# Kernel optimization log

Measured on AMD Instinct MI355X. Metric: run time of the kernel, lower is better.

Reference implementation:

```python
import jax, jax.numpy as jnp
import numpy as np

QLEN, MLEN, BSZ, DMODEL, NHEAD, DHEAD = 512, 512, 8, 1024, 16, 64
KLEN = QLEN + MLEN
LN_EPS = 1e-5


def layer_norm(x, g, b):
    mu = jnp.mean(x, axis=-1, keepdims=True)
    var = jnp.var(x, axis=-1, keepdims=True)
    return (x - mu) / jnp.sqrt(var + LN_EPS) * g + b


def rel_shift(x):
    # x: [qlen, klen, bsz, n_head] -- Transformer-XL relative shift trick
    q, k, b, n = x.shape
    x_pad = jnp.pad(x, ((0, 0), (1, 0), (0, 0), (0, 0)))  # zero col at front of dim 1
    x_pad = x_pad.reshape(k + 1, q, b, n)
    return x_pad[1:].reshape(q, k, b, n)


def setup_inputs() -> dict:
    key = jax.random.key(0)
    ks = jax.random.split(key, 10)
    w = lambda k, shape: (jax.random.normal(k, shape, jnp.float32) * 0.02)
    return {
        "content": jax.random.normal(ks[0], (QLEN, BSZ, DMODEL), jnp.float32),
        "mems": jax.random.normal(ks[1], (MLEN, BSZ, DMODEL), jnp.float32),
        "r": jax.random.normal(ks[2], (KLEN, DMODEL), jnp.float32),
        "q_bias": w(ks[3], (NHEAD, DHEAD)),
        "mask": jnp.zeros((QLEN, KLEN, BSZ), jnp.bool_),
        "W_q": w(ks[4], (NHEAD * DHEAD, DMODEL)),
        "W_kv": w(ks[5], (2 * NHEAD * DHEAD, DMODEL)),
        "W_r": w(ks[6], (NHEAD * DHEAD, DMODEL)),
        "b_r": jnp.zeros((NHEAD * DHEAD,), jnp.float32),
        "W_o": w(ks[7], (DMODEL, NHEAD * DHEAD)),
        "b_o": jnp.zeros((DMODEL,), jnp.float32),
        "ln_g": jnp.ones((DMODEL,), jnp.float32),
        "ln_b": jnp.zeros((DMODEL,), jnp.float32),
    }


def reference(content, mems, r, q_bias, mask, W_q, W_kv, W_r, b_r, W_o, b_o, ln_g, ln_b):
    Q, B, D = content.shape
    H, Dh = q_bias.shape
    scale = 1.0 / (Dh ** 0.5)

    c = layer_norm(content, ln_g, ln_b)          # [Q,B,D]
    m = layer_norm(mems, ln_g, ln_b)             # [M,B,D]
    cat = jnp.concatenate([m, c], axis=0)        # [K,B,D]
    K = cat.shape[0]

    kv = cat @ W_kv.T                            # [K,B,2*H*Dh]
    k, v = jnp.split(kv, 2, axis=-1)
    k = k.reshape(K, B, H, Dh)
    v = v.reshape(K, B, H, Dh)

    q = (c @ W_q.T).reshape(Q, B, H, Dh) + q_bias  # [Q,B,H,Dh]
    rproj = (r @ W_r.T + b_r).reshape(K, H, Dh)    # [K,H,Dh]

    AC = jnp.einsum('ibnd,jbnd->ijbn', q, k)       # content-content
    BD = rel_shift(jnp.einsum('ibnd,jnd->ijbn', q, rproj))  # content-position
    score = (AC + BD) * scale                      # [Q,K,B,H]
    score = jnp.where(mask[..., None], -jnp.inf, score)
    prob = jax.nn.softmax(score, axis=1)

    vec = jnp.einsum('ijbn,jbnd->ibnd', prob, v).reshape(Q, B, H * Dh)
    attn_out = vec @ W_o.T + b_o                   # [Q,B,D]
    # IdentityResidualGate: x + relu(y) with x = layer-normed content
    return c + jax.nn.relu(attn_out)
```

## Files before the change

### kernel.cpp

```cpp
#include <hip/hip_runtime.h>
#include <hip/hip_bf16.h>
#include <math.h>

#define QLEN 512
#define MLENC 512
#define KLEN 1024
#define BSZ 8
#define DMODEL 1024
#define NHEAD 16
#define DHEAD 64

typedef __hip_bfloat16 bf16;
typedef unsigned short u16;
typedef unsigned int u32;
typedef __attribute__((ext_vector_type(8))) short s16x8;
typedef __attribute__((ext_vector_type(4))) float f32x4;

#define MFMA16(a, b, c) __builtin_amdgcn_mfma_f32_16x16x32_bf16(a, b, c, 0, 0, 0)

static __device__ __forceinline__ float b2f(bf16 x) { return __bfloat162float(x); }
static __device__ __forceinline__ bf16 f2b(float x) { return __float2bfloat16(x); }
static __device__ __forceinline__ u16 bbu(float x) {
    bf16 h = __float2bfloat16(x);
    return *reinterpret_cast<u16*>(&h);
}
static __device__ __forceinline__ float sh2f(u16 v) {
    return __uint_as_float(((u32)v) << 16);
}

static __device__ __forceinline__ void gl_lds16(const void* g, void* l) {
    __builtin_amdgcn_global_load_lds(
        (const __attribute__((address_space(1))) void*)g,
        (__attribute__((address_space(3))) void*)l, 16, 0, 0);
}

__global__ __launch_bounds__(256) void wconv_kernel(const float* __restrict__ wq,
                                                    const float* __restrict__ wkv,
                                                    const float* __restrict__ wr,
                                                    const float* __restrict__ wo,
                                                    bf16* __restrict__ out) {
    int off = (blockIdx.x * 256 + threadIdx.x) * 8;
    const float* src;
    if (off < 1048576)       src = wq + off;
    else if (off < 3145728)  src = wkv + (off - 1048576);
    else if (off < 4194304)  src = wr + (off - 3145728);
    else                     src = wo + (off - 4194304);
    float4 f0 = *(const float4*)src;
    float4 f1 = *(const float4*)(src + 4);
    s16x8 v;
    v[0] = (short)bbu(f0.x); v[1] = (short)bbu(f0.y);
    v[2] = (short)bbu(f0.z); v[3] = (short)bbu(f0.w);
    v[4] = (short)bbu(f1.x); v[5] = (short)bbu(f1.y);
    v[6] = (short)bbu(f1.z); v[7] = (short)bbu(f1.w);
    *(s16x8*)((short*)out + off) = v;
}

__global__ __launch_bounds__(256) void ln_kernel(const float* __restrict__ content,
                                                 const float* __restrict__ mems,
                                                 const float* __restrict__ g,
                                                 const float* __restrict__ bet,
                                                 bf16* __restrict__ cat) {
    int row = blockIdx.x;
    int tid = threadIdx.x;
    const float* src = (row < MLENC * BSZ)
        ? mems + (size_t)row * DMODEL
        : content + (size_t)(row - MLENC * BSZ) * DMODEL;

    float x[4];
    float s = 0.f, ss = 0.f;
#pragma unroll
    for (int l = 0; l < 4; ++l) {
        int d = l * 256 + tid;
        x[l] = src[d];
        s += x[l];
        ss += x[l] * x[l];
    }
#pragma unroll
    for (int off = 32; off > 0; off >>= 1) {
        s  += __shfl_xor(s, off);
        ss += __shfl_xor(ss, off);
    }
    __shared__ float red[8];
    int wid = tid >> 6;
    if ((tid & 63) == 0) { red[wid * 2] = s; red[wid * 2 + 1] = ss; }
    __syncthreads();
    s  = red[0] + red[2] + red[4] + red[6];
    ss = red[1] + red[3] + red[5] + red[7];
    float mu  = s * (1.f / DMODEL);
    float var = ss * (1.f / DMODEL) - mu * mu;
    float rs  = rsqrtf(var + 1e-5f);
    bf16* dst = cat + (size_t)row * DMODEL;
#pragma unroll
    for (int l = 0; l < 4; ++l) {
        int d = l * 256 + tid;
        dst[d] = f2b((x[l] - mu) * rs * g[d] + bet[d]);
    }
}

template <int MODE, bool AF32, bool BF32>
__global__ __launch_bounds__(256) void gemm_mfma(const void* __restrict__ Av,
                                                 const void* __restrict__ Bv,
                                                 const float* __restrict__ bias,
                                                 const bf16* __restrict__ resid,
                                                 bf16* __restrict__ Cb,
                                                 float* __restrict__ Cf,
                                                 int Mr, int N) {
    __shared__ short As[128 * 32];
    __shared__ short Bs[128 * 32];

    int m0 = blockIdx.y * 128, n0 = blockIdx.x * 128;
    int tid = threadIdx.x;
    int w = tid >> 6, lane = tid & 63, l15 = lane & 15, quad = lane >> 4;
    int wm = w & 1, wn = w >> 1;

    const short* Ab = (const short*)Av;
    const float* Af = (const float*)Av;
    const short* Bb = (const short*)Bv;
    const float* Bf = (const float*)Bv;

    f32x4 acc[4][4];
#pragma unroll
    for (int i = 0; i < 4; ++i)
#pragma unroll
        for (int j = 0; j < 4; ++j) acc[i][j] = (f32x4){0.f, 0.f, 0.f, 0.f};

    for (int kt = 0; kt < 1024; kt += 32) {
        __syncthreads();
        if (!AF32) {
#pragma unroll
            for (int li = 0; li < 2; ++li) {
                int id = (li * 4 + w) * 64 + lane;
                int row = id >> 2, kc = (id & 3) * 8;
                gl_lds16(Ab + ((size_t)(m0 + row) * 1024 + kt + kc),
                         &As[(li * 4 + w) * 512]);
            }
        } else {
            int m = tid >> 1, kc = (tid & 1) * 16;
            const float* src = Af + (size_t)(m0 + m) * 1024 + kt + kc;
            u32* dst = (u32*)&As[m * 32 + kc];
#pragma unroll
            for (int q2 = 0; q2 < 4; ++q2) {
                float4 f = *(const float4*)(src + q2 * 4);
                dst[q2 * 2]     = ((u32)bbu(f.y) << 16) | bbu(f.x);
                dst[q2 * 2 + 1] = ((u32)bbu(f.w) << 16) | bbu(f.z);
            }
        }
        if (!BF32) {
#pragma unroll
            for (int li = 0; li < 2; ++li) {
                int id = (li * 4 + w) * 64 + lane;
                int row = id >> 2, kc = (id & 3) * 8;
                gl_lds16(Bb + ((size_t)(n0 + row) * 1024 + kt + kc),
                         &Bs[(li * 4 + w) * 512]);
            }
        } else {
            int nn = tid >> 1, kc = (tid & 1) * 16;
            const float* src = Bf + (size_t)(n0 + nn) * 1024 + kt + kc;
            u32* dst = (u32*)&Bs[nn * 32 + kc];
#pragma unroll
            for (int q2 = 0; q2 < 4; ++q2) {
                float4 f = *(const float4*)(src + q2 * 4);
                dst[q2 * 2]     = ((u32)bbu(f.y) << 16) | bbu(f.x);
                dst[q2 * 2 + 1] = ((u32)bbu(f.w) << 16) | bbu(f.z);
            }
        }
        __syncthreads();

        s16x8 af[4], bfr[4];
#pragma unroll
        for (int mb = 0; mb < 4; ++mb)
            af[mb] = *(const s16x8*)&As[(wm * 64 + mb * 16 + l15) * 32 + quad * 8];
#pragma unroll
        for (int nb = 0; nb < 4; ++nb)
            bfr[nb] = *(const s16x8*)&Bs[(wn * 64 + nb * 16 + l15) * 32 + quad * 8];
#pragma unroll
        for (int mb = 0; mb < 4; ++mb)
#pragma unroll
            for (int nb = 0; nb < 4; ++nb)
                acc[mb][nb] = MFMA16(af[mb], bfr[nb], acc[mb][nb]);
    }

#pragma unroll
    for (int mb = 0; mb < 4; ++mb) {
#pragma unroll
        for (int nb = 0; nb < 4; ++nb) {
#pragma unroll
            for (int r = 0; r < 4; ++r) {
                int m = m0 + wm * 64 + mb * 16 + quad * 4 + r;
                int col = n0 + wn * 64 + nb * 16 + l15;
                float v = acc[mb][nb][r];
                if (MODE >= 1) v += bias[col];
                if (MODE == 2) {
                    float rv = b2f(resid[(size_t)m * N + col]);
                    Cf[(size_t)m * N + col] = rv + fmaxf(v, 0.f);
                } else {
                    Cb[(size_t)m * N + col] = f2b(v);
                }
            }
        }
    }
}

template <int MODE, bool AF32, bool BF32>
__global__ __launch_bounds__(256) void gemm64(const void* __restrict__ Av,
                                              const void* __restrict__ Bv,
                                              const float* __restrict__ bias,
                                              const bf16* __restrict__ resid,
                                              bf16* __restrict__ Cb,
                                              float* __restrict__ Cf,
                                              int Mr, int N) {
    __shared__ short As[64 * 32];
    __shared__ short Bs[128 * 32];

    int m0 = blockIdx.y * 64, n0 = blockIdx.x * 128;
    int tid = threadIdx.x;
    int w = tid >> 6, lane = tid & 63, l15 = lane & 15, quad = lane >> 4;

    const short* Ab = (const short*)Av;
    const float* Af = (const float*)Av;
    const short* Bb = (const short*)Bv;
    const float* Bf = (const float*)Bv;

    f32x4 acc[4][2];
#pragma unroll
    for (int i = 0; i < 4; ++i)
#pragma unroll
        for (int j = 0; j < 2; ++j) acc[i][j] = (f32x4){0.f, 0.f, 0.f, 0.f};

    for (int kt = 0; kt < 1024; kt += 32) {
        __syncthreads();
        if (!AF32) {
            int id = w * 64 + lane;
            int row = id >> 2, kc = (id & 3) * 8;
            gl_lds16(Ab + ((size_t)(m0 + row) * 1024 + kt + kc), &As[w * 512]);
        } else {
            int m = tid >> 2, kc = (tid & 3) * 8;
            const float* src = Af + (size_t)(m0 + m) * 1024 + kt + kc;
            u32* dst = (u32*)&As[m * 32 + kc];
#pragma unroll
            for (int q2 = 0; q2 < 2; ++q2) {
                float4 f = *(const float4*)(src + q2 * 4);
                dst[q2 * 2]     = ((u32)bbu(f.y) << 16) | bbu(f.x);
                dst[q2 * 2 + 1] = ((u32)bbu(f.w) << 16) | bbu(f.z);
            }
        }
        if (!BF32) {
#pragma unroll
            for (int li = 0; li < 2; ++li) {
                int id = (li * 4 + w) * 64 + lane;
                int row = id >> 2, kc = (id & 3) * 8;
                gl_lds16(Bb + ((size_t)(n0 + row) * 1024 + kt + kc),
                         &Bs[(li * 4 + w) * 512]);
            }
        } else {
            int nn = tid >> 1, kc = (tid & 1) * 16;
            const float* src = Bf + (size_t)(n0 + nn) * 1024 + kt + kc;
            u32* dst = (u32*)&Bs[nn * 32 + kc];
#pragma unroll
            for (int q2 = 0; q2 < 4; ++q2) {
                float4 f = *(const float4*)(src + q2 * 4);
                dst[q2 * 2]     = ((u32)bbu(f.y) << 16) | bbu(f.x);
                dst[q2 * 2 + 1] = ((u32)bbu(f.w) << 16) | bbu(f.z);
            }
        }
        __syncthreads();

        s16x8 af[4], bfr[2];
#pragma unroll
        for (int mb = 0; mb < 4; ++mb)
            af[mb] = *(const s16x8*)&As[(mb * 16 + l15) * 32 + quad * 8];
#pragma unroll
        for (int nb = 0; nb < 2; ++nb)
            bfr[nb] = *(const s16x8*)&Bs[(w * 32 + nb * 16 + l15) * 32 + quad * 8];
#pragma unroll
        for (int mb = 0; mb < 4; ++mb)
#pragma unroll
            for (int nb = 0; nb < 2; ++nb)
                acc[mb][nb] = MFMA16(af[mb], bfr[nb], acc[mb][nb]);
    }

#pragma unroll
    for (int mb = 0; mb < 4; ++mb) {
#pragma unroll
        for (int nb = 0; nb < 2; ++nb) {
#pragma unroll
            for (int r = 0; r < 4; ++r) {
                int m = m0 + mb * 16 + quad * 4 + r;
                int col = n0 + w * 32 + nb * 16 + l15;
                float v = acc[mb][nb][r];
                if (MODE >= 1) v += bias[col];
                if (MODE == 2) {
                    float rv = b2f(resid[(size_t)m * N + col]);
                    Cf[(size_t)m * N + col] = rv + fmaxf(v, 0.f);
                } else {
                    Cb[(size_t)m * N + col] = f2b(v);
                }
            }
        }
    }
}

__global__ __launch_bounds__(256, 2) void attn_mfma(const bf16* __restrict__ qb,
                                                    const bf16* __restrict__ kv,
                                                    const bf16* __restrict__ rp,
                                                    bf16* __restrict__ vec) {
    __shared__ u16 Ks[64][72];
    __shared__ u16 Vr[2][4096];
    __shared__ u16 Vt[64][72];
    __shared__ u16 Ps[4][16][76];
    __shared__ u16 Ms[4][16][92];

    int bid = blockIdx.x;
    int it = bid & 7, n = (bid >> 3) & 15, b = bid >> 7;
    int i0 = it * 64;
    int tid = threadIdx.x;
    int w = tid >> 6, lane = tid & 63, l15 = lane & 15, quad = lane >> 4;

    const short* qs = (const short*)qb;
    const short* kvs = (const short*)kv;
    const short* rs = (const short*)rp;

    size_t qoff = (((size_t)(i0 + w * 16 + l15) * 8) + b) * 1024 + n * 64 + quad * 8;
    s16x8 aq0 = *(const s16x8*)(qs + qoff);
    s16x8 aq1 = *(const s16x8*)(qs + qoff + 32);
    int qrow1 = i0 + w * 16 + l15 + 1; if (qrow1 > 511) qrow1 = 511;
    size_t qoffs = (((size_t)qrow1 * 8) + b) * 1024 + n * 64 + quad * 8;
    s16x8 as0 = *(const s16x8*)(qs + qoffs);
    s16x8 as1 = *(const s16x8*)(qs + qoffs + 32);

    f32x4 O0 = {0.f,0.f,0.f,0.f}, O1 = O0, O2 = O0, O3 = O0;
    float mrun[4], lrun[4];
#pragma unroll
    for (int r = 0; r < 4; ++r) { mrun[r] = -INFINITY; lrun[r] = 0.f; }

    f32x4 z = (f32x4){0.f, 0.f, 0.f, 0.f};
    int ibase = i0 + w * 16 + quad * 4;

    int r0K = tid >> 3, c0K = (tid & 7) * 8;
    int dV = lane, jV = w * 16;
    int wrow = (3 - w) * 16 + l15;

    auto loadW = [&](int ubase, s16x8* dst) {
#pragma unroll
        for (int ntl = 0; ntl < 5; ++ntl) {
            int u = ubase + wrow + ntl * 16;
            u = u < 0 ? 0 : (u > 1023 ? 1023 : u);
            const short* p = rs + (size_t)u * 1024 + n * 64 + quad * 8;
            dst[ntl * 2]     = *(const s16x8*)p;
            dst[ntl * 2 + 1] = *(const s16x8*)(p + 32);
        }
    };
    auto bandM = [&](const s16x8* wf, s16x8 a0, s16x8 a1, f32x4* th) {
        f32x4 m[5];
#pragma unroll
        for (int ntl = 0; ntl < 5; ++ntl) {
            m[ntl] = MFMA16(a0, wf[ntl * 2], z);
            m[ntl] = MFMA16(a1, wf[ntl * 2 + 1], m[ntl]);
        }
#pragma unroll
        for (int ntl = 0; ntl < 5; ++ntl)
#pragma unroll
            for (int r = 0; r < 4; ++r)
                Ms[w][quad * 4 + r][ntl * 16 + l15] = bbu(m[ntl][r]);
        __asm__ __volatile__("s_waitcnt lgkmcnt(0)" ::: "memory");
#pragma unroll
        for (int r = 0; r < 4; ++r) {
            int lr = quad * 4 + r;
            int cb = l15 - lr + 15;
#pragma unroll
            for (int h = 0; h < 4; ++h)
                th[h][r] = sh2f(Ms[w][lr][cb + 16 * h]);
        }
        __asm__ __volatile__("s_waitcnt lgkmcnt(0)" ::: "memory");
    };

    {
        size_t base0 = ((size_t)(r0K * 8 + b)) * 2048 + n * 64 + c0K;
        size_t base1 = ((size_t)((32 + r0K) * 8 + b)) * 2048 + n * 64 + c0K;
        s16x8 k0 = *(const s16x8*)(kvs + base0);
        s16x8 k1 = *(const s16x8*)(kvs + base1);
        gl_lds16(kvs + base0 + 1024, &Vr[0][w * 512]);
        gl_lds16(kvs + base1 + 1024, &Vr[0][2048 + w * 512]);
        *(s16x8*)&Ks[r0K][c0K] = k0;
        *(s16x8*)&Ks[32 + r0K][c0K] = k1;
    }

    for (int st = 0; st < 16; ++st) {
        int p = st & 1;
        int j0 = st * 64;
        int d0 = j0 - i0;
        int j0n = (j0 + 64) & 1023;

        __syncthreads();

        bool need1 = (d0 <= 512);
        bool need2 = (d0 >= 512);
        s16x8 wf1[10];
        if (need1) loadW(448 + d0, wf1);

        size_t base0 = ((size_t)((j0n + r0K) * 8 + b)) * 2048 + n * 64 + c0K;
        size_t base1 = ((size_t)((j0n + 32 + r0K) * 8 + b)) * 2048 + n * 64 + c0K;
        s16x8 kr0 = *(const s16x8*)(kvs + base0);
        s16x8 kr1 = *(const s16x8*)(kvs + base1);
        gl_lds16(kvs + base0 + 1024, &Vr[1 - p][w * 512]);
        gl_lds16(kvs + base1 + 1024, &Vr[1 - p][2048 + w * 512]);

        {
            s16x8 vv0, vv1;
#pragma unroll
            for (int q2 = 0; q2 < 8; ++q2) vv0[q2] = (short)Vr[p][(jV + q2) * 64 + dV];
#pragma unroll
            for (int q2 = 0; q2 < 8; ++q2) vv1[q2] = (short)Vr[p][(jV + 8 + q2) * 64 + dV];
            *(s16x8*)&Vt[dV][jV] = vv0;
            *(s16x8*)&Vt[dV][jV + 8] = vv1;
        }

        f32x4 sc[4];
#pragma unroll
        for (int h = 0; h < 4; ++h) {
            s16x8 bk0 = *(const s16x8*)&Ks[h * 16 + l15][quad * 8];
            s16x8 bk1 = *(const s16x8*)&Ks[h * 16 + l15][32 + quad * 8];
            sc[h] = MFMA16(aq0, bk0, z);
            sc[h] = MFMA16(aq1, bk1, sc[h]);
        }

        f32x4 th1[4], th2[4];
#pragma unroll
        for (int h = 0; h < 4; ++h) { th1[h] = z; th2[h] = z; }
        if (need1) bandM(wf1, aq0, aq1, th1);
        if (need2) {
            s16x8 wf2[10];
            loadW(d0 - 577, wf2);
            bandM(wf2, as0, as1, th2);
        }

#pragma unroll
        for (int r = 0; r < 4; ++r) {
            int rr = w * 16 + quad * 4 + r;
            int djb = j0 + l15 - i0 - rr;
#pragma unroll
            for (int h = 0; h < 4; ++h) {
                int dj = djb + 16 * h;
                float bd = (dj <= 512) ? th1[h][r] : ((dj == 513) ? 0.f : th2[h][r]);
                sc[h][r] = (sc[h][r] + bd) * 0.125f;
            }
        }

#pragma unroll
        for (int r = 0; r < 4; ++r) {
            float ml = fmaxf(fmaxf(sc[0][r], sc[1][r]), fmaxf(sc[2][r], sc[3][r]));
            ml = fmaxf(ml, __shfl_xor(ml, 1));
            ml = fmaxf(ml, __shfl_xor(ml, 2));
            ml = fmaxf(ml, __shfl_xor(ml, 4));
            ml = fmaxf(ml, __shfl_xor(ml, 8));
            float mn = fmaxf(mrun[r], ml);
            float p0 = __expf(sc[0][r] - mn);
            float p1 = __expf(sc[1][r] - mn);
            float p2 = __expf(sc[2][r] - mn);
            float p3 = __expf(sc[3][r] - mn);
            float ps = (p0 + p1) + (p2 + p3);
            ps += __shfl_xor(ps, 1);
            ps += __shfl_xor(ps, 2);
            ps += __shfl_xor(ps, 4);
            ps += __shfl_xor(ps, 8);
            float al = __expf(mrun[r] - mn);
            lrun[r] = lrun[r] * al + ps;
            mrun[r] = mn;
            O0[r] *= al; O1[r] *= al; O2[r] *= al; O3[r] *= al;
            int lr = quad * 4 + r;
            Ps[w][lr][l15]      = bbu(p0);
            Ps[w][lr][16 + l15] = bbu(p1);
            Ps[w][lr][32 + l15] = bbu(p2);
            Ps[w][lr][48 + l15] = bbu(p3);
        }

        __syncthreads();

        s16x8 ap0 = *(const s16x8*)&Ps[w][l15][quad * 8];
        s16x8 ap1 = *(const s16x8*)&Ps[w][l15][32 + quad * 8];
        {
            s16x8 bv0 = *(const s16x8*)&Vt[l15][quad * 8];
            s16x8 bv1 = *(const s16x8*)&Vt[l15][32 + quad * 8];
            O0 = MFMA16(ap0, bv0, O0);
            O0 = MFMA16(ap1, bv1, O0);
        }
        {
            s16x8 bv0 = *(const s16x8*)&Vt[16 + l15][quad * 8];
            s16x8 bv1 = *(const s16x8*)&Vt[16 + l15][32 + quad * 8];
            O1 = MFMA16(ap0, bv0, O1);
            O1 = MFMA16(ap1, bv1, O1);
        }
        {
            s16x8 bv0 = *(const s16x8*)&Vt[32 + l15][quad * 8];
            s16x8 bv1 = *(const s16x8*)&Vt[32 + l15][32 + quad * 8];
            O2 = MFMA16(ap0, bv0, O2);
            O2 = MFMA16(ap1, bv1, O2);
        }
        {
            s16x8 bv0 = *(const s16x8*)&Vt[48 + l15][quad * 8];
            s16x8 bv1 = *(const s16x8*)&Vt[48 + l15][32 + quad * 8];
            O3 = MFMA16(ap0, bv0, O3);
            O3 = MFMA16(ap1, bv1, O3);
        }

        *(s16x8*)&Ks[r0K][c0K] = kr0;
        *(s16x8*)&Ks[32 + r0K][c0K] = kr1;
    }

#pragma unroll
    for (int r = 0; r < 4; ++r) {
        float inv = 1.f / lrun[r];
        int ig = ibase + r;
        size_t o = ((size_t)ig * 8 + b) * 1024 + n * 64;
        vec[o + l15]      = f2b(O0[r] * inv);
        vec[o + 16 + l15] = f2b(O1[r] * inv);
        vec[o + 32 + l15] = f2b(O2[r] * inv);
        vec[o + 48 + l15] = f2b(O3[r] * inv);
    }
}

extern "C" void kernel_launch(void* const* d_in, const int* in_sizes, int n_in,
                              void* d_out, int out_size, void* d_ws, size_t ws_size,
                              hipStream_t stream) {
    const float* content = (const float*)d_in[0];
    const float* mems    = (const float*)d_in[1];
    const float* r       = (const float*)d_in[2];
    const float* q_bias  = (const float*)d_in[3];
    const float* W_q     = (const float*)d_in[5];
    const float* W_kv    = (const float*)d_in[6];
    const float* W_r     = (const float*)d_in[7];
    const float* b_r     = (const float*)d_in[8];
    const float* W_o     = (const float*)d_in[9];
    const float* b_o     = (const float*)d_in[10];
    const float* ln_g    = (const float*)d_in[11];
    const float* ln_b    = (const float*)d_in[12];

    bf16* ws   = (bf16*)d_ws;
    bf16* cat  = ws;
    bf16* kv   = cat + 8388608;
    bf16* qb   = kv + 16777216;
    bf16* rp   = qb + 4194304;
    bf16* vecb = rp + 1048576;
    bf16* Wb   = vecb + 4194304;
    bf16* catc = cat + (size_t)MLENC * BSZ * DMODEL;

    bf16* Wqb  = Wb;
    bf16* Wkvb = Wb + 1048576;
    bf16* Wrb  = Wb + 3145728;
    bf16* Wob  = Wb + 4194304;

    const size_t FULLW_BYTES = (size_t)(34603008 + 5242880) * 2;
    bool fullw = ws_size >= FULLW_BYTES;

    ln_kernel<<<KLEN * BSZ, 256, 0, stream>>>(content, mems, ln_g, ln_b, cat);

    if (fullw) {
        wconv_kernel<<<2560, 256, 0, stream>>>(W_q, W_kv, W_r, W_o, Wb);

        gemm_mfma<0, false, false><<<dim3(16, 64), 256, 0, stream>>>(
            cat, Wkvb, nullptr, nullptr, kv, nullptr, 8192, 2048);
        gemm64<1, false, false><<<dim3(8, 64), 256, 0, stream>>>(
            catc, Wqb, q_bias, nullptr, qb, nullptr, 4096, 1024);
        gemm64<1, true, false><<<dim3(8, 16), 256, 0, stream>>>(
            r, Wrb, b_r, nullptr, rp, nullptr, 1024, 1024);
    } else {
        gemm_mfma<0, false, true><<<dim3(16, 64), 256, 0, stream>>>(
            cat, W_kv, nullptr, nullptr, kv, nullptr, 8192, 2048);
        gemm64<1, false, true><<<dim3(8, 64), 256, 0, stream>>>(
            catc, W_q, q_bias, nullptr, qb, nullptr, 4096, 1024);
        gemm64<1, true, true><<<dim3(8, 16), 256, 0, stream>>>(
            r, W_r, b_r, nullptr, rp, nullptr, 1024, 1024);
    }

    attn_mfma<<<BSZ * NHEAD * 8, 256, 0, stream>>>(qb, kv, rp, vecb);

    if (fullw) {
        gemm64<2, false, false><<<dim3(8, 64), 256, 0, stream>>>(
            vecb, Wob, b_o, catc, nullptr, (float*)d_out, 4096, 1024);
    } else {
        gemm64<2, false, true><<<dim3(8, 64), 256, 0, stream>>>(
            vecb, W_o, b_o, catc, nullptr, (float*)d_out, 4096, 1024);
    }
}
```

Baseline: 378.1 us.

## Cut attention LDS use and raise occupancy with shuffles, register V prefetch, MFMA row sums

The attention kernel drops the Vr staging buffer and the Ms band scratch buffer. The relative-shift band extraction now uses cross-lane shuffles instead of an LDS round trip. V is prefetched into registers with scalar 16-bit global loads, and softmax row sums are accumulated with an MFMA against a ones vector instead of shuffle reductions. Launch bounds go from 2 to 4 blocks per SIMD to exploit the smaller LDS footprint. The cost is uncoalesced 2-byte V loads, more register pressure, and row sums computed from bf16-rounded probabilities.

```diff
diff --git a/kernel.cpp b/kernel.cpp
--- a/kernel.cpp
+++ b/kernel.cpp
@@ -23,9 +23,6 @@
 static __device__ __forceinline__ u16 bbu(float x) {
     bf16 h = __float2bfloat16(x);
     return *reinterpret_cast<u16*>(&h);
-}
-static __device__ __forceinline__ float sh2f(u16 v) {
-    return __uint_as_float(((u32)v) << 16);
 }
 
 static __device__ __forceinline__ void gl_lds16(const void* g, void* l) {
@@ -300,15 +297,13 @@
     }
 }
 
-__global__ __launch_bounds__(256, 2) void attn_mfma(const bf16* __restrict__ qb,
+__global__ __launch_bounds__(256, 4) void attn_mfma(const bf16* __restrict__ qb,
                                                     const bf16* __restrict__ kv,
                                                     const bf16* __restrict__ rp,
                                                     bf16* __restrict__ vec) {
     __shared__ u16 Ks[64][72];
-    __shared__ u16 Vr[2][4096];
     __shared__ u16 Vt[64][72];
     __shared__ u16 Ps[4][16][76];
-    __shared__ u16 Ms[4][16][92];
 
     int bid = blockIdx.x;
     int it = bid & 7, n = (bid >> 3) & 15, b = bid >> 7;
@@ -318,6 +313,7 @@
 
     const short* qs = (const short*)qb;
     const short* kvs = (const short*)kv;
+    const u16* kvu = (const u16*)kv;
     const short* rs = (const short*)rp;
 
     size_t qoff = (((size_t)(i0 + w * 16 + l15) * 8) + b) * 1024 + n * 64 + quad * 8;
@@ -329,12 +325,17 @@
     s16x8 as1 = *(const s16x8*)(qs + qoffs + 32);
 
     f32x4 O0 = {0.f,0.f,0.f,0.f}, O1 = O0, O2 = O0, O3 = O0;
-    float mrun[4], lrun[4];
-#pragma unroll
-    for (int r = 0; r < 4; ++r) { mrun[r] = -INFINITY; lrun[r] = 0.f; }
+    f32x4 Lacc = O0;
+    float mrun[4];
+#pragma unroll
+    for (int r = 0; r < 4; ++r) mrun[r] = -INFINITY;
 
     f32x4 z = (f32x4){0.f, 0.f, 0.f, 0.f};
     int ibase = i0 + w * 16 + quad * 4;
+
+    s16x8 ones;
+#pragma unroll
+    for (int i = 0; i < 8; ++i) ones[i] = (short)0x3F80;
 
     int r0K = tid >> 3, c0K = (tid & 7) * 8;
     int dV = lane, jV = w * 16;
@@ -358,62 +359,67 @@
             m[ntl] = MFMA16(a1, wf[ntl * 2 + 1], m[ntl]);
         }
 #pragma unroll
-        for (int ntl = 0; ntl < 5; ++ntl)
-#pragma unroll
-            for (int r = 0; r < 4; ++r)
-                Ms[w][quad * 4 + r][ntl * 16 + l15] = bbu(m[ntl][r]);
-        __asm__ __volatile__("s_waitcnt lgkmcnt(0)" ::: "memory");
-#pragma unroll
         for (int r = 0; r < 4; ++r) {
             int lr = quad * 4 + r;
             int cb = l15 - lr + 15;
-#pragma unroll
-            for (int h = 0; h < 4; ++h)
-                th[h][r] = sh2f(Ms[w][lr][cb + 16 * h]);
-        }
-        __asm__ __volatile__("s_waitcnt lgkmcnt(0)" ::: "memory");
+            int sidx = quad * 16 + (cb & 15);
+            float s0v = __shfl(m[0][r], sidx);
+            float s1v = __shfl(m[1][r], sidx);
+            float s2v = __shfl(m[2][r], sidx);
+            float s3v = __shfl(m[3][r], sidx);
+            float s4v = __shfl(m[4][r], sidx);
+            bool hi = cb >= 16;
+            th[0][r] = hi ? s1v : s0v;
+            th[1][r] = hi ? s2v : s1v;
+            th[2][r] = hi ? s3v : s2v;
+            th[3][r] = hi ? s4v : s3v;
+        }
     };
 
+    u16 vbuf[16];
     {
         size_t base0 = ((size_t)(r0K * 8 + b)) * 2048 + n * 64 + c0K;
         size_t base1 = ((size_t)((32 + r0K) * 8 + b)) * 2048 + n * 64 + c0K;
         s16x8 k0 = *(const s16x8*)(kvs + base0);
         s16x8 k1 = *(const s16x8*)(kvs + base1);
-        gl_lds16(kvs + base0 + 1024, &Vr[0][w * 512]);
-        gl_lds16(kvs + base1 + 1024, &Vr[0][2048 + w * 512]);
         *(s16x8*)&Ks[r0K][c0K] = k0;
         *(s16x8*)&Ks[32 + r0K][c0K] = k1;
+        size_t vb = ((size_t)(jV * 8 + b)) * 2048 + 1024 + n * 64 + dV;
+#pragma unroll
+        for (int q2 = 0; q2 < 16; ++q2)
+            vbuf[q2] = kvu[vb + (size_t)q2 * 16384];
     }
 
     for (int st = 0; st < 16; ++st) {
-        int p = st & 1;
         int j0 = st * 64;
         int d0 = j0 - i0;
         int j0n = (j0 + 64) & 1023;
 
         __syncthreads();
+
+        {
+            s16x8 vv0, vv1;
+#pragma unroll
+            for (int q2 = 0; q2 < 8; ++q2) { vv0[q2] = (short)vbuf[q2]; vv1[q2] = (short)vbuf[8 + q2]; }
+            *(s16x8*)&Vt[dV][jV] = vv0;
+            *(s16x8*)&Vt[dV][jV + 8] = vv1;
+        }
+
+        {
+            size_t vb = ((size_t)((j0n + jV) * 8 + b)) * 2048 + 1024 + n * 64 + dV;
+#pragma unroll
+            for (int q2 = 0; q2 < 16; ++q2)
+                vbuf[q2] = kvu[vb + (size_t)q2 * 16384];
+        }
+        size_t base0 = ((size_t)((j0n + r0K) * 8 + b)) * 2048 + n * 64 + c0K;
+        size_t base1 = ((size_t)((j0n + 32 + r0K) * 8 + b)) * 2048 + n * 64 + c0K;
+        s16x8 kr0 = *(const s16x8*)(kvs + base0);
+        s16x8 kr1 = *(const s16x8*)(kvs + base1);
 
         bool need1 = (d0 <= 512);
         bool need2 = (d0 >= 512);
         s16x8 wf1[10];
         if (need1) loadW(448 + d0, wf1);
-
-        size_t base0 = ((size_t)((j0n + r0K) * 8 + b)) * 2048 + n * 64 + c0K;
-        size_t base1 = ((size_t)((j0n + 32 + r0K) * 8 + b)) * 2048 + n * 64 + c0K;
-        s16x8 kr0 = *(const s16x8*)(kvs + base0);
-        s16x8 kr1 = *(const s16x8*)(kvs + base1);
-        gl_lds16(kvs + base0 + 1024, &Vr[1 - p][w * 512]);
-        gl_lds16(kvs + base1 + 1024, &Vr[1 - p][2048 + w * 512]);
-
-        {
-            s16x8 vv0, vv1;
-#pragma unroll
-            for (int q2 = 0; q2 < 8; ++q2) vv0[q2] = (short)Vr[p][(jV + q2) * 64 + dV];
-#pragma unroll
-            for (int q2 = 0; q2 < 8; ++q2) vv1[q2] = (short)Vr[p][(jV + 8 + q2) * 64 + dV];
-            *(s16x8*)&Vt[dV][jV] = vv0;
-            *(s16x8*)&Vt[dV][jV + 8] = vv1;
-        }
 
         f32x4 sc[4];
 #pragma unroll
@@ -458,14 +464,9 @@
             float p1 = __expf(sc[1][r] - mn);
             float p2 = __expf(sc[2][r] - mn);
             float p3 = __expf(sc[3][r] - mn);
-            float ps = (p0 + p1) + (p2 + p3);
-            ps += __shfl_xor(ps, 1);
-            ps += __shfl_xor(ps, 2);
-            ps += __shfl_xor(ps, 4);
-            ps += __shfl_xor(ps, 8);
             float al = __expf(mrun[r] - mn);
-            lrun[r] = lrun[r] * al + ps;
             mrun[r] = mn;
+            Lacc[r] *= al;
             O0[r] *= al; O1[r] *= al; O2[r] *= al; O3[r] *= al;
             int lr = quad * 4 + r;
             Ps[w][lr][l15]      = bbu(p0);
@@ -502,6 +503,8 @@
             O3 = MFMA16(ap0, bv0, O3);
             O3 = MFMA16(ap1, bv1, O3);
         }
+        Lacc = MFMA16(ap0, ones, Lacc);
+        Lacc = MFMA16(ap1, ones, Lacc);
 
         *(s16x8*)&Ks[r0K][c0K] = kr0;
         *(s16x8*)&Ks[32 + r0K][c0K] = kr1;
@@ -509,7 +512,7 @@
 
 #pragma unroll
     for (int r = 0; r < 4; ++r) {
-        float inv = 1.f / lrun[r];
+        float inv = 1.f / Lacc[r];
         int ig = ibase + r;
         size_t o = ((size_t)ig * 8 + b) * 1024 + n * 64;
         vec[o + l15]      = f2b(O0[r] * inv);
```

Result: slower. 604.3 us (+59.8%).

## Prefetch next step's relative-position weights and keep band scratch in fp32

Applied to the files above, without the earlier changes.

The relative-position (rproj) fragments for the next key tile are now loaded from global memory one step ahead into ping-pong register buffers, so the band-matrix MFMA no longer waits on that load. The loop is manually unrolled by two to alternate the buffers. The band scratch in LDS is changed from bf16 to fp32, which removes the conversion and the explicit waitcnt barriers but uses more LDS. Register pressure rises from the extra 10-vector prefetch buffer, which could affect occupancy at two blocks per SM.

```diff
diff --git a/kernel.cpp b/kernel.cpp
--- a/kernel.cpp
+++ b/kernel.cpp
@@ -23,9 +23,6 @@
 static __device__ __forceinline__ u16 bbu(float x) {
     bf16 h = __float2bfloat16(x);
     return *reinterpret_cast<u16*>(&h);
-}
-static __device__ __forceinline__ float sh2f(u16 v) {
-    return __uint_as_float(((u32)v) << 16);
 }
 
 static __device__ __forceinline__ void gl_lds16(const void* g, void* l) {
@@ -308,7 +305,7 @@
     __shared__ u16 Vr[2][4096];
     __shared__ u16 Vt[64][72];
     __shared__ u16 Ps[4][16][76];
-    __shared__ u16 Ms[4][16][92];
+    __shared__ float Ms[4][16][84];
 
     int bid = blockIdx.x;
     int it = bid & 7, n = (bid >> 3) & 15, b = bid >> 7;
@@ -361,42 +358,25 @@
         for (int ntl = 0; ntl < 5; ++ntl)
 #pragma unroll
             for (int r = 0; r < 4; ++r)
-                Ms[w][quad * 4 + r][ntl * 16 + l15] = bbu(m[ntl][r]);
-        __asm__ __volatile__("s_waitcnt lgkmcnt(0)" ::: "memory");
+                Ms[w][quad * 4 + r][ntl * 16 + l15] = m[ntl][r];
 #pragma unroll
         for (int r = 0; r < 4; ++r) {
             int lr = quad * 4 + r;
             int cb = l15 - lr + 15;
 #pragma unroll
             for (int h = 0; h < 4; ++h)
-                th[h][r] = sh2f(Ms[w][lr][cb + 16 * h]);
-        }
-        __asm__ __volatile__("s_waitcnt lgkmcnt(0)" ::: "memory");
+                th[h][r] = Ms[w][lr][cb + 16 * h];
+        }
     };
 
-    {
-        size_t base0 = ((size_t)(r0K * 8 + b)) * 2048 + n * 64 + c0K;
-        size_t base1 = ((size_t)((32 + r0K) * 8 + b)) * 2048 + n * 64 + c0K;
-        s16x8 k0 = *(const s16x8*)(kvs + base0);
-        s16x8 k1 = *(const s16x8*)(kvs + base1);
-        gl_lds16(kvs + base0 + 1024, &Vr[0][w * 512]);
-        gl_lds16(kvs + base1 + 1024, &Vr[0][2048 + w * 512]);
-        *(s16x8*)&Ks[r0K][c0K] = k0;
-        *(s16x8*)&Ks[32 + r0K][c0K] = k1;
-    }
-
-    for (int st = 0; st < 16; ++st) {
+    bool need1c, need2c;
+    auto step = [&](int st, s16x8* wcur, s16x8* wnxt) {
         int p = st & 1;
         int j0 = st * 64;
         int d0 = j0 - i0;
         int j0n = (j0 + 64) & 1023;
 
         __syncthreads();
-
-        bool need1 = (d0 <= 512);
-        bool need2 = (d0 >= 512);
-        s16x8 wf1[10];
-        if (need1) loadW(448 + d0, wf1);
 
         size_t base0 = ((size_t)((j0n + r0K) * 8 + b)) * 2048 + n * 64 + c0K;
         size_t base1 = ((size_t)((j0n + 32 + r0K) * 8 + b)) * 2048 + n * 64 + c0K;
@@ -405,6 +385,11 @@
         gl_lds16(kvs + base0 + 1024, &Vr[1 - p][w * 512]);
         gl_lds16(kvs + base1 + 1024, &Vr[1 - p][2048 + w * 512]);
 
+        int d0p = d0 + 64;
+        bool need1n = (d0p <= 512);
+        bool need2n = (d0p >= 512);
+        loadW(need1n ? (448 + d0p) : (d0p - 577), wnxt);
+
         {
             s16x8 vv0, vv1;
 #pragma unroll
@@ -427,11 +412,15 @@
         f32x4 th1[4], th2[4];
 #pragma unroll
         for (int h = 0; h < 4; ++h) { th1[h] = z; th2[h] = z; }
-        if (need1) bandM(wf1, aq0, aq1, th1);
-        if (need2) {
-            s16x8 wf2[10];
-            loadW(d0 - 577, wf2);
-            bandM(wf2, as0, as1, th2);
+        if (need1c) bandM(wcur, aq0, aq1, th1);
+        if (need2c) {
+            if (need1c) {
+                s16x8 w2[10];
+                loadW(d0 - 577, w2);
+                bandM(w2, as0, as1, th2);
+            } else {
+                bandM(wcur, as0, as1, th2);
+            }
         }
 
 #pragma unroll
@@ -505,6 +494,28 @@
 
         *(s16x8*)&Ks[r0K][c0K] = kr0;
         *(s16x8*)&Ks[32 + r0K][c0K] = kr1;
+        need1c = need1n;
+        need2c = need2n;
+    };
+
+    s16x8 wA[10], wB[10];
+    {
+        size_t base0 = ((size_t)(r0K * 8 + b)) * 2048 + n * 64 + c0K;
+        size_t base1 = ((size_t)((32 + r0K) * 8 + b)) * 2048 + n * 64 + c0K;
+        s16x8 k0 = *(const s16x8*)(kvs + base0);
+        s16x8 k1 = *(const s16x8*)(kvs + base1);
+        gl_lds16(kvs + base0 + 1024, &Vr[0][w * 512]);
+        gl_lds16(kvs + base1 + 1024, &Vr[0][2048 + w * 512]);
+        *(s16x8*)&Ks[r0K][c0K] = k0;
+        *(s16x8*)&Ks[32 + r0K][c0K] = k1;
+        loadW(448 - i0, wA);
+        need1c = true;
+        need2c = (-i0 >= 512);
+    }
+
+    for (int st2 = 0; st2 < 16; st2 += 2) {
+        step(st2,     wA, wB);
+        step(st2 + 1, wB, wA);
     }
 
 #pragma unroll
```

Result: no change. 371.0 us (-1.9%).
